# Kernel optimization log

Measured on AMD Instinct MI355X. Metric: run time of the kernel, lower is better.

Reference implementation:

```python
import jax, jax.numpy as jnp
import numpy as np

EPS = 1e-12  # matches torch F.normalize default eps

def _l2norm(x, axis):
    n = jnp.sqrt(jnp.sum(x * x, axis=axis, keepdims=True))
    return x / jnp.maximum(n, EPS)

def setup_inputs() -> dict:
    key = jax.random.key(0)
    k1, k2, k3 = jax.random.split(key, 3)
    bs, V, N = 2, 4096, 32
    S, K = 8, 64
    neighbor_index = jax.random.randint(k1, (bs, V, N), 0, V)
    vertices = jax.random.normal(k2, (bs, V, 3), dtype=jnp.float32)
    directions = jax.random.normal(k3, (3, S * K), dtype=jnp.float32) * (1.0 / np.sqrt(S * K))
    return {"neighbor_index": neighbor_index, "vertices": vertices, "directions": directions}

def reference(neighbor_index, vertices, directions):
    # neighbor_index: (bs, V, N) int; vertices: (bs, V, 3); directions: (3, S*K)
    bs, V, N = neighbor_index.shape
    S, K = 8, 64
    id0 = jnp.arange(bs)[:, None, None]
    neighbors = vertices[id0, neighbor_index]                    # (bs, V, N, 3) gather
    nd = _l2norm(neighbors - vertices[:, :, None, :], axis=-1)   # (bs, V, N, 3)
    sd = _l2norm(directions, axis=0)                             # (3, S*K)
    theta = jax.nn.relu(jnp.einsum('bvnd,dm->bvnm', nd, sd))     # (bs, V, N, S*K)
    theta = theta.reshape(bs, V, N, S, K)
    theta = jnp.max(theta, axis=2)                               # max over neighbors
    feature = jnp.sum(theta, axis=2)                             # sum over supports -> (bs, V, K)
    return feature
```

## Files before the change

kernel.cpp:

```cpp
#include <hip/hip_runtime.h>

#define BS 2
#define V_DIM 4096
#define N_NBR 32
#define S_SUP 8
#define K_OUT 64
#define SK (S_SUP * K_OUT)
#define WAVES_PER_BLOCK 4

typedef float f32x2 __attribute__((ext_vector_type(2)));
typedef float f32x4 __attribute__((ext_vector_type(4)));

__global__ __launch_bounds__(WAVES_PER_BLOCK * 64, 8) void conv_surface_kernel(
    const int* __restrict__ nidx,
    const float* __restrict__ verts,
    const float* __restrict__ dirs,
    float* __restrict__ out)
{
    const int lane = threadIdx.x & 63;
    const int wave = threadIdx.x >> 6;
    const int vi   = blockIdx.x * WAVES_PER_BLOCK + wave;
    const int bbase = (vi >> 12) << 12;

    __shared__ __align__(16) float snd[WAVES_PER_BLOCK][N_NBR][4];

    int j = 0;
    if (lane < N_NBR) j = nidx[vi * N_NBR + lane];
    const float cx = verts[vi * 3 + 0];
    const float cy = verts[vi * 3 + 1];
    const float cz = verts[vi * 3 + 2];

    float a0[S_SUP], a1[S_SUP], a2[S_SUP];
#pragma unroll
    for (int s = 0; s < S_SUP; ++s) {
        const int m = s * K_OUT + lane;
        a0[s] = dirs[0 * SK + m];
        a1[s] = dirs[1 * SK + m];
        a2[s] = dirs[2 * SK + m];
    }

    if (lane < N_NBR) {
        const float dx = verts[(bbase + j) * 3 + 0] - cx;
        const float dy = verts[(bbase + j) * 3 + 1] - cy;
        const float dz = verts[(bbase + j) * 3 + 2] - cz;
        const float inv = __frsqrt_rn(fmaxf(dx * dx + dy * dy + dz * dz, 1e-24f));
        f32x4 q = {dx * inv, dy * inv, dz * inv, 0.0f};
        *reinterpret_cast<f32x4*>(&snd[wave][lane][0]) = q;
    }

    f32x2 D0[S_SUP / 2], D1[S_SUP / 2], D2[S_SUP / 2];
#pragma unroll
    for (int p = 0; p < S_SUP / 2; ++p) {
        const int s0 = 2 * p, s1 = 2 * p + 1;
        const float i0 = __frsqrt_rn(fmaxf(a0[s0]*a0[s0] + a1[s0]*a1[s0] + a2[s0]*a2[s0], 1e-24f));
        const float i1 = __frsqrt_rn(fmaxf(a0[s1]*a0[s1] + a1[s1]*a1[s1] + a2[s1]*a2[s1], 1e-24f));
        D0[p] = (f32x2){a0[s0] * i0, a0[s1] * i1};
        D1[p] = (f32x2){a1[s0] * i0, a1[s1] * i1};
        D2[p] = (f32x2){a2[s0] * i0, a2[s1] * i1};
    }

    f32x2 th[S_SUP / 2];
#pragma unroll
    for (int p = 0; p < S_SUP / 2; ++p) th[p] = (f32x2){0.0f, 0.0f};

#pragma unroll 4
    for (int n = 0; n < N_NBR; ++n) {
        const f32x4 q = *reinterpret_cast<const f32x4*>(&snd[wave][n][0]);
        const f32x2 vx = (f32x2){q.x, q.x};
        const f32x2 vy = (f32x2){q.y, q.y};
        const f32x2 vz = (f32x2){q.z, q.z};
#pragma unroll
        for (int p = 0; p < S_SUP / 2; ++p) {
            f32x2 t = vx * D0[p];
            t = t + vy * D1[p];
            t = t + vz * D2[p];
            th[p] = __builtin_elementwise_max(th[p], t);
        }
    }

    const f32x2 u = th[0] + th[1];
    const f32x2 w = th[2] + th[3];
    const f32x2 z = u + w;
    out[vi * K_OUT + lane] = z.x + z.y;
}

extern "C" void kernel_launch(void* const* d_in, const int* in_sizes, int n_in,
                              void* d_out, int out_size, void* d_ws, size_t ws_size,
                              hipStream_t stream) {
    const int*   nidx  = (const int*)d_in[0];
    const float* verts = (const float*)d_in[1];
    const float* dirs  = (const float*)d_in[2];
    float*       out   = (float*)d_out;

    const int total_v = BS * V_DIM;
    const int blocks  = total_v / WAVES_PER_BLOCK;
    conv_surface_kernel<<<blocks, WAVES_PER_BLOCK * 64, 0, stream>>>(nidx, verts, dirs, out);
}
```

Baseline: 16.19 us.

## Process two vertices per wave to reuse normalized directions and fill all lanes

Each wave now handles two vertices. The two half-waves each gather and normalize the 32 neighbors of one vertex, so all 64 lanes do work during the gather phase. The direction loading and normalization cost is paid once per pair of vertices, and the launch uses half as many blocks. The neighbor loop is fully unrolled, and the launch-bounds occupancy hint is removed, which may raise register pressure and lower occupancy.

```diff
diff --git a/kernel.cpp b/kernel.cpp
--- a/kernel.cpp
+++ b/kernel.cpp
@@ -7,11 +7,12 @@
 #define K_OUT 64
 #define SK (S_SUP * K_OUT)
 #define WAVES_PER_BLOCK 4
+#define VPW 2
 
 typedef float f32x2 __attribute__((ext_vector_type(2)));
 typedef float f32x4 __attribute__((ext_vector_type(4)));
 
-__global__ __launch_bounds__(WAVES_PER_BLOCK * 64, 8) void conv_surface_kernel(
+__global__ __launch_bounds__(WAVES_PER_BLOCK * 64) void conv_surface_kernel(
     const int* __restrict__ nidx,
     const float* __restrict__ verts,
     const float* __restrict__ dirs,
@@ -19,16 +20,19 @@
 {
     const int lane = threadIdx.x & 63;
     const int wave = threadIdx.x >> 6;
-    const int vi   = blockIdx.x * WAVES_PER_BLOCK + wave;
-    const int bbase = (vi >> 12) << 12;
+    const int v0   = (blockIdx.x * WAVES_PER_BLOCK + wave) * VPW;
 
-    __shared__ __align__(16) float snd[WAVES_PER_BLOCK][N_NBR][4];
+    const int h  = lane >> 5;
+    const int ln = lane & 31;
+    const int vg = v0 + h;
+    const int bbase = (vg >> 12) << 12;
 
-    int j = 0;
-    if (lane < N_NBR) j = nidx[vi * N_NBR + lane];
-    const float cx = verts[vi * 3 + 0];
-    const float cy = verts[vi * 3 + 1];
-    const float cz = verts[vi * 3 + 2];
+    __shared__ __align__(16) float snd[WAVES_PER_BLOCK][VPW][N_NBR][4];
+
+    const int j = nidx[vg * N_NBR + ln];
+    const float cx = verts[vg * 3 + 0];
+    const float cy = verts[vg * 3 + 1];
+    const float cz = verts[vg * 3 + 2];
 
     float a0[S_SUP], a1[S_SUP], a2[S_SUP];
 #pragma unroll
@@ -39,13 +43,13 @@
         a2[s] = dirs[2 * SK + m];
     }
 
-    if (lane < N_NBR) {
+    {
         const float dx = verts[(bbase + j) * 3 + 0] - cx;
         const float dy = verts[(bbase + j) * 3 + 1] - cy;
         const float dz = verts[(bbase + j) * 3 + 2] - cz;
         const float inv = __frsqrt_rn(fmaxf(dx * dx + dy * dy + dz * dz, 1e-24f));
         f32x4 q = {dx * inv, dy * inv, dz * inv, 0.0f};
-        *reinterpret_cast<f32x4*>(&snd[wave][lane][0]) = q;
+        *reinterpret_cast<f32x4*>(&snd[wave][h][ln][0]) = q;
     }
 
     f32x2 D0[S_SUP / 2], D1[S_SUP / 2], D2[S_SUP / 2];
@@ -59,29 +63,32 @@
         D2[p] = (f32x2){a2[s0] * i0, a2[s1] * i1};
     }
 
-    f32x2 th[S_SUP / 2];
 #pragma unroll
-    for (int p = 0; p < S_SUP / 2; ++p) th[p] = (f32x2){0.0f, 0.0f};
+    for (int v = 0; v < VPW; ++v) {
+        f32x2 th[S_SUP / 2];
+#pragma unroll
+        for (int p = 0; p < S_SUP / 2; ++p) th[p] = (f32x2){0.0f, 0.0f};
 
-#pragma unroll 4
-    for (int n = 0; n < N_NBR; ++n) {
-        const f32x4 q = *reinterpret_cast<const f32x4*>(&snd[wave][n][0]);
-        const f32x2 vx = (f32x2){q.x, q.x};
-        const f32x2 vy = (f32x2){q.y, q.y};
-        const f32x2 vz = (f32x2){q.z, q.z};
 #pragma unroll
-        for (int p = 0; p < S_SUP / 2; ++p) {
-            f32x2 t = vx * D0[p];
-            t = t + vy * D1[p];
-            t = t + vz * D2[p];
-            th[p] = __builtin_elementwise_max(th[p], t);
+        for (int n = 0; n < N_NBR; ++n) {
+            const f32x4 q = *reinterpret_cast<const f32x4*>(&snd[wave][v][n][0]);
+            const f32x2 vx = (f32x2){q.x, q.x};
+            const f32x2 vy = (f32x2){q.y, q.y};
+            const f32x2 vz = (f32x2){q.z, q.z};
+#pragma unroll
+            for (int p = 0; p < S_SUP / 2; ++p) {
+                f32x2 t = vx * D0[p];
+                t = t + vy * D1[p];
+                t = t + vz * D2[p];
+                th[p] = __builtin_elementwise_max(th[p], t);
+            }
         }
+
+        const f32x2 u = th[0] + th[1];
+        const f32x2 w = th[2] + th[3];
+        const f32x2 z = u + w;
+        out[(v0 + v) * K_OUT + lane] = z.x + z.y;
     }
-
-    const f32x2 u = th[0] + th[1];
-    const f32x2 w = th[2] + th[3];
-    const f32x2 z = u + w;
-    out[vi * K_OUT + lane] = z.x + z.y;
 }
 
 extern "C" void kernel_launch(void* const* d_in, const int* in_sizes, int n_in,
@@ -93,6 +100,6 @@
     float*       out   = (float*)d_out;
 
     const int total_v = BS * V_DIM;
-    const int blocks  = total_v / WAVES_PER_BLOCK;
+    const int blocks  = total_v / (WAVES_PER_BLOCK * VPW);
     conv_surface_kernel<<<blocks, WAVES_PER_BLOCK * 64, 0, stream>>>(nidx, verts, dirs, out);
 }
```

Measured after the change: 15.40 us (median of 2 runs). 1.05x faster.
